# Kernel tuning notes

Measured on AMD Instinct MI355X. Metric: run time of the kernel, lower is better.

## Reference

```python
import jax, jax.numpy as jnp
import numpy as np

# ---- Clifford algebra Cl(3,0): 8 blades ordered by grade: [1, e1,e2,e3, e12,e13,e23, e123] ----
_ORDER = [0, 1, 2, 4, 3, 5, 6, 7]  # bitmask of each blade in grade-sorted order
GRADES = np.array([0, 1, 1, 1, 2, 2, 2, 3])  # grade (subspace) of each blade
EPS = 1e-6

def _build_cayley():
    C = np.zeros((8, 8, 8), np.float32)
    for ia, a in enumerate(_ORDER):
        for ib, b in enumerate(_ORDER):
            # reordering sign from anticommuting basis vectors (Euclidean metric -> squares +1)
            t, tot = a >> 1, 0
            while t:
                tot += bin(t & b).count("1")
                t >>= 1
            s = 1.0 if tot % 2 == 0 else -1.0
            C[ia, ib, _ORDER.index(a ^ b)] = s
    return jnp.asarray(C)

CAYLEY = _build_cayley()  # [8,8,8], highly sparse (64 nonzeros)

def mvlinear(x, W, b):
    # x: [B,N,Cin,8], W: [Cout,Cin,4] per-grade weights, b: [Cout] bias on scalar blade
    Wf = W[:, :, GRADES]                               # [Cout,Cin,8] via repeat over grades [1,3,3,1]
    y = jnp.einsum("bnci,oci->bnoi", x, Wf)
    return y.at[..., 0].add(b)

def setup_inputs() -> dict:
    key = jax.random.key(0)
    ks = jax.random.split(key, 5)
    B, N, Cin, Ch = 8, 4096, 64, 128
    return {
        "x": jax.random.normal(ks[0], (B, N, Cin, 8), jnp.float32),
        "W1": jax.random.normal(ks[1], (Ch, Cin, 4), jnp.float32) / np.sqrt(Cin),
        "b1": jax.random.normal(ks[2], (Ch,), jnp.float32) * 0.02,
        "W2": jax.random.normal(ks[3], (Cin, Ch, 4), jnp.float32) / np.sqrt(Ch),
        "b2": jax.random.normal(ks[4], (Cin,), jnp.float32) * 0.02,
        "a": jnp.ones((Cin,), jnp.float32),
    }

def reference(x, W1, b1, W2, b2, a):
    h = mvlinear(x, W1, b1)                                   # [B,N,Ch,8]
    h = jnp.einsum("bnci,ijk,bncj->bnck", h, CAYLEY, h)       # geometric product (sparse Cayley)
    y = mvlinear(h, W2, b2)                                   # [B,N,Cin,8]
    # MVLayerNorm: per-channel multivector norm (Euclidean: sqrt(sum of squares)),
    # averaged over channels, then scale by learned a
    norm = jnp.sqrt(jnp.sum(y * y, axis=-1, keepdims=True))   # [B,N,Cin,1]
    denom = jnp.mean(norm, axis=-2, keepdims=True) + EPS      # [B,N,1,1]
    return a[None, None, :, None] * y / denom
```

## Files before the change

### kernel.cpp

```cpp
#include <hip/hip_runtime.h>
#include <stdint.h>

typedef unsigned short u16;
typedef __attribute__((ext_vector_type(4))) float f32x4;
typedef __attribute__((ext_vector_type(8))) __bf16 bf16x8;

#define XPITCH 72
#define GPITCH 136

struct Cay { int idx[8][8]; float sgn[8][8]; };
constexpr int kOrder[8] = {0,1,2,4,3,5,6,7};
constexpr int ordpos(int m){ int r=-1; for(int i=0;i<8;i++) if(kOrder[i]==m) r=i; return r; }
constexpr Cay make_cay(){
  Cay c{};
  for(int ia=0; ia<8; ia++) for(int ib=0; ib<8; ib++){
    int a=kOrder[ia], b=kOrder[ib];
    int t=a>>1, tot=0;
    while(t){ int x=t&b; while(x){ tot+=x&1; x>>=1; } t>>=1; }
    c.idx[ia][ib]=ordpos(a^b);
    c.sgn[ia][ib]=(tot&1)?-1.0f:1.0f;
  }
  return c;
}
constexpr Cay CAY = make_cay();

__device__ __forceinline__ u16 f2bf(float f){
  union { float f; uint32_t u; } v; v.f=f;
  uint32_t u=v.u;
  return (u16)((u + 0x7fffu + ((u>>16)&1u)) >> 16);
}

__global__ void gp_prepack(const float* __restrict__ W1, const float* __restrict__ W2,
                           u16* __restrict__ w1p, u16* __restrict__ w2p)
{
  int t = blockIdx.x*256 + threadIdx.x;
  int e = t & 7, l = (t>>3)&63, f = t>>9;
  int lm = l & 15, lh = l >> 4;
  if (f < 64) {
    int g = f >> 4, ks = (f>>3)&1, ot = f&7;
    int o = ot*16 + lm, c = ks*32 + lh*8 + e;
    w1p[f*512 + l*8 + e] = f2bf(W1[(o*64 + c)*4 + g]);
  } else {
    int f2 = f - 64;
    int g = f2 >> 4, ks = (f2>>2)&3, ot = f2&3;
    int outc = ot*16 + lm, o = ks*32 + lh*8 + e;
    w2p[f2*512 + l*8 + e] = f2bf(W2[(outc*128 + o)*4 + g]);
  }
}

__global__ __launch_bounds__(512,4) void gp_fused(
    const float* __restrict__ x, const u16* __restrict__ w1p,
    const float* __restrict__ b1, const u16* __restrict__ w2p,
    const float* __restrict__ b2, const float* __restrict__ avec,
    float* __restrict__ out)
{
  __shared__ u16 SH[8*32*GPITCH];
  __shared__ float redArr[32][4];
  __shared__ float denomArr[32];

  const int tid = threadIdx.x;
  const int w  = tid >> 6;
  const int l  = tid & 63;
  const int lm = l & 15;
  const int lh = l >> 4;

  {
    const float4* x4 = reinterpret_cast<const float4*>(x) + (size_t)blockIdx.x * 4096;
    #pragma unroll
    for (int it = 0; it < 8; ++it) {
      int q = it*512 + tid;
      float4 v = x4[q];
      int i0 = (q & 1) * 4;
      int c  = (q >> 1) & 63;
      int p  = q >> 7;
      SH[((i0+0)*32 + p)*XPITCH + c] = f2bf(v.x);
      SH[((i0+1)*32 + p)*XPITCH + c] = f2bf(v.y);
      SH[((i0+2)*32 + p)*XPITCH + c] = f2bf(v.z);
      SH[((i0+3)*32 + p)*XPITCH + c] = f2bf(v.w);
    }
  }
  __syncthreads();

  constexpr int BSTART[4] = {0,1,4,7};
  constexpr int BCNT[4]   = {1,3,3,1};

  f32x4 acc1[2][8];
  #pragma unroll
  for (int pt=0; pt<2; ++pt)
    #pragma unroll
    for (int b=0; b<8; ++b)
      acc1[pt][b] = (f32x4){0.f,0.f,0.f,0.f};

  const uint4* w1f = reinterpret_cast<const uint4*>(w1p);
  #pragma unroll
  for (int g=0; g<4; ++g) {
    #pragma unroll
    for (int ks=0; ks<2; ++ks) {
      uint4 bu = w1f[(((g*2+ks)*8 + w)*64) + l];
      bf16x8 bv = __builtin_bit_cast(bf16x8, bu);
      #pragma unroll
      for (int bi=0; bi<3; ++bi) {
        if (bi >= BCNT[g]) break;
        const int blade = BSTART[g] + bi;
        #pragma unroll
        for (int pt=0; pt<2; ++pt) {
          uint4 au = *reinterpret_cast<const uint4*>(
              &SH[((blade*32 + pt*16 + lm)*XPITCH) + ks*32 + lh*8]);
          bf16x8 av = __builtin_bit_cast(bf16x8, au);
          acc1[pt][blade] = __builtin_amdgcn_mfma_f32_16x16x32_bf16(av, bv, acc1[pt][blade], 0,0,0);
        }
      }
    }
  }
  __syncthreads();

  {
    const float b1v = b1[w*16 + lm];
    #pragma unroll
    for (int pt=0; pt<2; ++pt) {
      #pragma unroll
      for (int r=0; r<4; ++r) {
        float h[8];
        #pragma unroll
        for (int b=0; b<8; ++b) h[b] = acc1[pt][b][r];
        h[0] += b1v;
        float gg[8] = {0,0,0,0,0,0,0,0};
        #pragma unroll
        for (int i=0; i<8; ++i)
          #pragma unroll
          for (int j=0; j<8; ++j)
            gg[CAY.idx[i][j]] += CAY.sgn[i][j] * h[i] * h[j];
        const int pos = pt*16 + lh*4 + r;
        #pragma unroll
        for (int b=0; b<8; ++b)
          SH[(b*32 + pos)*GPITCH + w*16 + lm] = f2bf(gg[b]);
      }
    }
  }
  __syncthreads();

  const int pt2 = w >> 2;
  const int ot2 = w & 3;
  f32x4 acc2[8];
  #pragma unroll
  for (int b=0; b<8; ++b) acc2[b] = (f32x4){0.f,0.f,0.f,0.f};

  const uint4* w2f = reinterpret_cast<const uint4*>(w2p);
  #pragma unroll
  for (int ks=0; ks<4; ++ks) {
    #pragma unroll
    for (int g=0; g<4; ++g) {
      uint4 bu = w2f[(((g*4+ks)*4 + ot2)*64) + l];
      bf16x8 bv = __builtin_bit_cast(bf16x8, bu);
      #pragma unroll
      for (int bi=0; bi<3; ++bi) {
        if (bi >= BCNT[g]) break;
        const int blade = BSTART[g] + bi;
        uint4 au = *reinterpret_cast<const uint4*>(
            &SH[((blade*32 + pt2*16 + lm)*GPITCH) + ks*32 + lh*8]);
        bf16x8 av = __builtin_bit_cast(bf16x8, au);
        acc2[blade] = __builtin_amdgcn_mfma_f32_16x16x32_bf16(av, bv, acc2[blade], 0,0,0);
      }
    }
  }

  const float b2v  = b2[ot2*16 + lm];
  const float aval = avec[ot2*16 + lm];
  #pragma unroll
  for (int r=0; r<4; ++r) acc2[0][r] += b2v;

  float nrm[4];
  #pragma unroll
  for (int r=0; r<4; ++r) {
    float s = 0.f;
    #pragma unroll
    for (int b=0; b<8; ++b) s += acc2[b][r]*acc2[b][r];
    nrm[r] = sqrtf(s);
  }
  #pragma unroll
  for (int r=0; r<4; ++r) {
    float v = nrm[r];
    v += __shfl_xor(v, 1, 64);
    v += __shfl_xor(v, 2, 64);
    v += __shfl_xor(v, 4, 64);
    v += __shfl_xor(v, 8, 64);
    nrm[r] = v;
  }
  if (lm == 0) {
    #pragma unroll
    for (int r=0; r<4; ++r) redArr[pt2*16 + lh*4 + r][ot2] = nrm[r];
  }
  __syncthreads();
  if (tid < 32)
    denomArr[tid] = (redArr[tid][0]+redArr[tid][1]+redArr[tid][2]+redArr[tid][3])
                    * (1.0f/64.0f) + 1e-6f;
  __syncthreads();

  #pragma unroll
  for (int r=0; r<4; ++r) {
    const int pos = pt2*16 + lh*4 + r;
    const float sc = aval / denomArr[pos];
    float4 o0, o1;
    o0.x = acc2[0][r]*sc; o0.y = acc2[1][r]*sc; o0.z = acc2[2][r]*sc; o0.w = acc2[3][r]*sc;
    o1.x = acc2[4][r]*sc; o1.y = acc2[5][r]*sc; o1.z = acc2[6][r]*sc; o1.w = acc2[7][r]*sc;
    size_t P = (size_t)blockIdx.x*32 + pos;
    float4* op = reinterpret_cast<float4*>(out + (P*64 + (size_t)(ot2*16+lm))*8);
    op[0] = o0; op[1] = o1;
  }
}

extern "C" void kernel_launch(void* const* d_in, const int* in_sizes, int n_in,
                              void* d_out, int out_size, void* d_ws, size_t ws_size,
                              hipStream_t stream)
{
  const float* x  = (const float*)d_in[0];
  const float* W1 = (const float*)d_in[1];
  const float* b1 = (const float*)d_in[2];
  const float* W2 = (const float*)d_in[3];
  const float* b2 = (const float*)d_in[4];
  const float* a  = (const float*)d_in[5];
  float* out = (float*)d_out;

  u16* w1p = (u16*)d_ws;
  u16* w2p = w1p + 32768;

  gp_prepack<<<256, 256, 0, stream>>>(W1, W2, w1p, w2p);
  gp_fused<<<1024, 512, 0, stream>>>(x, w1p, b1, w2p, b2, a, out);
}
```

Before: 47.87 us.

## Halve block tile to 16 points, XOR-swizzle LDS, symmetric geometric product

Each block now handles 16 points with 256 threads instead of 32 points with 512, and the grid doubles to compensate. The padded LDS pitches are replaced with an XOR-swizzled layout. The first GEMM is transposed so one LDS activation fragment feeds two MFMAs with different weight tiles. The geometric product exploits symmetric Cayley pairs to cut multiply count, and bf16 conversion uses packed v_cvt_pk_bf16_f32 with vectorized LDS stores. These changes target LDS bank conflicts, conversion overhead and ALU work in the Cayley step, at the cost of smaller tiles and more per-block weight reloads.

```diff
diff --git a/kernel.cpp b/kernel.cpp
--- a/kernel.cpp
+++ b/kernel.cpp
@@ -4,9 +4,6 @@
 typedef unsigned short u16;
 typedef __attribute__((ext_vector_type(4))) float f32x4;
 typedef __attribute__((ext_vector_type(8))) __bf16 bf16x8;
-
-#define XPITCH 72
-#define GPITCH 136
 
 struct Cay { int idx[8][8]; float sgn[8][8]; };
 constexpr int kOrder[8] = {0,1,2,4,3,5,6,7};
@@ -24,10 +21,41 @@
 }
 constexpr Cay CAY = make_cay();
 
+struct GPTab { float dsgn[8]; int np; int pi[28]; int pj[28]; int pk[28]; float ps[28]; };
+constexpr GPTab make_gptab(){
+  GPTab t{};
+  for (int i=0;i<8;i++) t.dsgn[i] = CAY.sgn[i][i];
+  t.np = 0;
+  for (int i=0;i<8;i++) for (int j=i+1;j<8;j++){
+    float s = CAY.sgn[i][j] + CAY.sgn[j][i];
+    if (s != 0.0f){ t.pi[t.np]=i; t.pj[t.np]=j; t.pk[t.np]=CAY.idx[i][j]; t.ps[t.np]=s; t.np++; }
+  }
+  return t;
+}
+constexpr GPTab GPT = make_gptab();
+
+__device__ __forceinline__ void gprod(const float* h, float* g){
+  float g0 = h[0]*h[0];
+  #pragma unroll
+  for (int i=1;i<8;i++) g0 = fmaf(GPT.dsgn[i]>0.f ? h[i] : -h[i], h[i], g0);
+  g[0] = g0;
+  #pragma unroll
+  for (int k=1;k<8;k++) g[k] = 0.f;
+  #pragma unroll
+  for (int t=0;t<GPT.np;t++)
+    g[GPT.pk[t]] = fmaf(GPT.ps[t]*h[GPT.pi[t]], h[GPT.pj[t]], g[GPT.pk[t]]);
+}
+
 __device__ __forceinline__ u16 f2bf(float f){
   union { float f; uint32_t u; } v; v.f=f;
   uint32_t u=v.u;
   return (u16)((u + 0x7fffu + ((u>>16)&1u)) >> 16);
+}
+
+__device__ __forceinline__ uint32_t cvtpk(float lo, float hi){
+  uint32_t r;
+  asm("v_cvt_pk_bf16_f32 %0, %1, %2" : "=v"(r) : "v"(lo), "v"(hi));
+  return r;
 }
 
 __global__ void gp_prepack(const float* __restrict__ W1, const float* __restrict__ W2,
@@ -48,35 +76,39 @@
   }
 }
 
-__global__ __launch_bounds__(512,4) void gp_fused(
+__global__ __launch_bounds__(256,4) void gp_fused(
     const float* __restrict__ x, const u16* __restrict__ w1p,
     const float* __restrict__ b1, const u16* __restrict__ w2p,
     const float* __restrict__ b2, const float* __restrict__ avec,
     float* __restrict__ out)
 {
-  __shared__ u16 SH[8*32*GPITCH];
-  __shared__ float redArr[32][4];
-  __shared__ float denomArr[32];
+  __shared__ __align__(16) char SH[32768];
+  __shared__ float redArr[16][4];
+  __shared__ float denomArr[16];
 
   const int tid = threadIdx.x;
   const int w  = tid >> 6;
   const int l  = tid & 63;
   const int lm = l & 15;
   const int lh = l >> 4;
+  const int xk = (lm & 7) << 4;
 
   {
-    const float4* x4 = reinterpret_cast<const float4*>(x) + (size_t)blockIdx.x * 4096;
-    #pragma unroll
-    for (int it = 0; it < 8; ++it) {
-      int q = it*512 + tid;
-      float4 v = x4[q];
-      int i0 = (q & 1) * 4;
-      int c  = (q >> 1) & 63;
-      int p  = q >> 7;
-      SH[((i0+0)*32 + p)*XPITCH + c] = f2bf(v.x);
-      SH[((i0+1)*32 + p)*XPITCH + c] = f2bf(v.y);
-      SH[((i0+2)*32 + p)*XPITCH + c] = f2bf(v.z);
-      SH[((i0+3)*32 + p)*XPITCH + c] = f2bf(v.w);
+    const int cp = tid & 31;
+    const int pr = tid >> 5;
+    const float4* xt = reinterpret_cast<const float4*>(x) + (size_t)blockIdx.x * 2048;
+    #pragma unroll
+    for (int it=0; it<2; ++it){
+      const int p = pr + it*8;
+      const float4* src = xt + p*128 + cp*4;
+      float4 v0 = src[0], v1 = src[1], v2 = src[2], v3 = src[3];
+      uint32_t pk[8];
+      pk[0]=cvtpk(v0.x,v2.x); pk[1]=cvtpk(v0.y,v2.y); pk[2]=cvtpk(v0.z,v2.z); pk[3]=cvtpk(v0.w,v2.w);
+      pk[4]=cvtpk(v1.x,v3.x); pk[5]=cvtpk(v1.y,v3.y); pk[6]=cvtpk(v1.z,v3.z); pk[7]=cvtpk(v1.w,v3.w);
+      const int xo = (p & 7) << 4;
+      #pragma unroll
+      for (int b=0;b<8;b++)
+        *reinterpret_cast<uint32_t*>(SH + ((((p*8+b)<<7) + (cp<<2)) ^ xo)) = pk[b];
     }
   }
   __syncthreads();
@@ -86,86 +118,96 @@
 
   f32x4 acc1[2][8];
   #pragma unroll
-  for (int pt=0; pt<2; ++pt)
+  for (int cc=0; cc<2; ++cc)
     #pragma unroll
     for (int b=0; b<8; ++b)
-      acc1[pt][b] = (f32x4){0.f,0.f,0.f,0.f};
+      acc1[cc][b] = (f32x4){0.f,0.f,0.f,0.f};
 
   const uint4* w1f = reinterpret_cast<const uint4*>(w1p);
   #pragma unroll
-  for (int g=0; g<4; ++g) {
-    #pragma unroll
-    for (int ks=0; ks<2; ++ks) {
-      uint4 bu = w1f[(((g*2+ks)*8 + w)*64) + l];
-      bf16x8 bv = __builtin_bit_cast(bf16x8, bu);
-      #pragma unroll
-      for (int bi=0; bi<3; ++bi) {
-        if (bi >= BCNT[g]) break;
-        const int blade = BSTART[g] + bi;
-        #pragma unroll
-        for (int pt=0; pt<2; ++pt) {
-          uint4 au = *reinterpret_cast<const uint4*>(
-              &SH[((blade*32 + pt*16 + lm)*XPITCH) + ks*32 + lh*8]);
-          bf16x8 av = __builtin_bit_cast(bf16x8, au);
-          acc1[pt][blade] = __builtin_amdgcn_mfma_f32_16x16x32_bf16(av, bv, acc1[pt][blade], 0,0,0);
-        }
-      }
-    }
-  }
-  __syncthreads();
-
-  {
-    const float b1v = b1[w*16 + lm];
-    #pragma unroll
-    for (int pt=0; pt<2; ++pt) {
-      #pragma unroll
-      for (int r=0; r<4; ++r) {
+  for (int g4=0; g4<4; ++g4){
+    #pragma unroll
+    for (int ks=0; ks<2; ++ks){
+      uint4 wa = w1f[((g4*2+ks)*8 + w    )*64 + l];
+      uint4 wb = w1f[((g4*2+ks)*8 + w + 4)*64 + l];
+      bf16x8 wav = __builtin_bit_cast(bf16x8, wa);
+      bf16x8 wbv = __builtin_bit_cast(bf16x8, wb);
+      #pragma unroll
+      for (int bi=0; bi<3; ++bi){
+        if (bi >= BCNT[g4]) break;
+        const int blade = BSTART[g4] + bi;
+        bf16x8 xv = *reinterpret_cast<const bf16x8*>(
+            SH + ((((lm*8+blade)<<7) + ((ks*32+lh*8)<<1)) ^ xk));
+        acc1[0][blade] = __builtin_amdgcn_mfma_f32_16x16x32_bf16(wav, xv, acc1[0][blade], 0,0,0);
+        acc1[1][blade] = __builtin_amdgcn_mfma_f32_16x16x32_bf16(wbv, xv, acc1[1][blade], 0,0,0);
+      }
+    }
+  }
+  __syncthreads();
+
+  #pragma unroll
+  for (int cc=0; cc<2; ++cc){
+    const int cht = w + cc*4;
+    const float4 b14 = reinterpret_cast<const float4*>(b1)[cht*4 + lh];
+    const float bb[4] = {b14.x, b14.y, b14.z, b14.w};
+    uint32_t lo[8], hi[8];
+    #pragma unroll
+    for (int rp=0; rp<2; ++rp){
+      float ga[8], gb[8];
+      {
         float h[8];
         #pragma unroll
-        for (int b=0; b<8; ++b) h[b] = acc1[pt][b][r];
-        h[0] += b1v;
-        float gg[8] = {0,0,0,0,0,0,0,0};
+        for (int b=0;b<8;b++) h[b] = acc1[cc][b][rp*2+0];
+        h[0] += bb[rp*2+0];
+        gprod(h, ga);
+      }
+      {
+        float h[8];
         #pragma unroll
-        for (int i=0; i<8; ++i)
-          #pragma unroll
-          for (int j=0; j<8; ++j)
-            gg[CAY.idx[i][j]] += CAY.sgn[i][j] * h[i] * h[j];
-        const int pos = pt*16 + lh*4 + r;
-        #pragma unroll
-        for (int b=0; b<8; ++b)
-          SH[(b*32 + pos)*GPITCH + w*16 + lm] = f2bf(gg[b]);
-      }
-    }
-  }
-  __syncthreads();
-
-  const int pt2 = w >> 2;
-  const int ot2 = w & 3;
+        for (int b=0;b<8;b++) h[b] = acc1[cc][b][rp*2+1];
+        h[0] += bb[rp*2+1];
+        gprod(h, gb);
+      }
+      #pragma unroll
+      for (int b=0;b<8;b++){
+        uint32_t v = cvtpk(ga[b], gb[b]);
+        if (rp==0) lo[b] = v; else hi[b] = v;
+      }
+    }
+    const int chByte = (cht*16 + lh*4) << 1;
+    #pragma unroll
+    for (int b=0;b<8;b++){
+      uint2 v; v.x = lo[b]; v.y = hi[b];
+      *reinterpret_cast<uint2*>(SH + ((((lm*8+b)<<8) + chByte) ^ xk)) = v;
+    }
+  }
+  __syncthreads();
+
   f32x4 acc2[8];
   #pragma unroll
   for (int b=0; b<8; ++b) acc2[b] = (f32x4){0.f,0.f,0.f,0.f};
 
   const uint4* w2f = reinterpret_cast<const uint4*>(w2p);
   #pragma unroll
-  for (int ks=0; ks<4; ++ks) {
-    #pragma unroll
-    for (int g=0; g<4; ++g) {
-      uint4 bu = w2f[(((g*4+ks)*4 + ot2)*64) + l];
-      bf16x8 bv = __builtin_bit_cast(bf16x8, bu);
-      #pragma unroll
-      for (int bi=0; bi<3; ++bi) {
-        if (bi >= BCNT[g]) break;
-        const int blade = BSTART[g] + bi;
-        uint4 au = *reinterpret_cast<const uint4*>(
-            &SH[((blade*32 + pt2*16 + lm)*GPITCH) + ks*32 + lh*8]);
-        bf16x8 av = __builtin_bit_cast(bf16x8, au);
-        acc2[blade] = __builtin_amdgcn_mfma_f32_16x16x32_bf16(av, bv, acc2[blade], 0,0,0);
-      }
-    }
-  }
-
-  const float b2v  = b2[ot2*16 + lm];
-  const float aval = avec[ot2*16 + lm];
+  for (int ks=0; ks<4; ++ks){
+    #pragma unroll
+    for (int g4=0; g4<4; ++g4){
+      uint4 wu = w2f[((g4*4+ks)*4 + w)*64 + l];
+      bf16x8 wv = __builtin_bit_cast(bf16x8, wu);
+      #pragma unroll
+      for (int bi=0; bi<3; ++bi){
+        if (bi >= BCNT[g4]) break;
+        const int blade = BSTART[g4] + bi;
+        bf16x8 gv = *reinterpret_cast<const bf16x8*>(
+            SH + ((((lm*8+blade)<<8) + ((ks*32+lh*8)<<1)) ^ xk));
+        acc2[blade] = __builtin_amdgcn_mfma_f32_16x16x32_bf16(gv, wv, acc2[blade], 0,0,0);
+      }
+    }
+  }
+
+  const int oc = w*16 + lm;
+  const float b2v  = b2[oc];
+  const float aval = avec[oc];
   #pragma unroll
   for (int r=0; r<4; ++r) acc2[0][r] += b2v;
 
@@ -174,7 +216,7 @@
   for (int r=0; r<4; ++r) {
     float s = 0.f;
     #pragma unroll
-    for (int b=0; b<8; ++b) s += acc2[b][r]*acc2[b][r];
+    for (int b=0; b<8; ++b) s = fmaf(acc2[b][r], acc2[b][r], s);
     nrm[r] = sqrtf(s);
   }
   #pragma unroll
@@ -188,23 +230,23 @@
   }
   if (lm == 0) {
     #pragma unroll
-    for (int r=0; r<4; ++r) redArr[pt2*16 + lh*4 + r][ot2] = nrm[r];
-  }
-  __syncthreads();
-  if (tid < 32)
+    for (int r=0; r<4; ++r) redArr[lh*4 + r][w] = nrm[r];
+  }
+  __syncthreads();
+  if (tid < 16)
     denomArr[tid] = (redArr[tid][0]+redArr[tid][1]+redArr[tid][2]+redArr[tid][3])
                     * (1.0f/64.0f) + 1e-6f;
   __syncthreads();
 
   #pragma unroll
   for (int r=0; r<4; ++r) {
-    const int pos = pt2*16 + lh*4 + r;
+    const int pos = lh*4 + r;
     const float sc = aval / denomArr[pos];
     float4 o0, o1;
     o0.x = acc2[0][r]*sc; o0.y = acc2[1][r]*sc; o0.z = acc2[2][r]*sc; o0.w = acc2[3][r]*sc;
     o1.x = acc2[4][r]*sc; o1.y = acc2[5][r]*sc; o1.z = acc2[6][r]*sc; o1.w = acc2[7][r]*sc;
-    size_t P = (size_t)blockIdx.x*32 + pos;
-    float4* op = reinterpret_cast<float4*>(out + (P*64 + (size_t)(ot2*16+lm))*8);
+    size_t P = (size_t)blockIdx.x*16 + pos;
+    float4* op = reinterpret_cast<float4*>(out + (P*64 + (size_t)oc)*8);
     op[0] = o0; op[1] = o1;
   }
 }
@@ -225,5 +267,5 @@
   u16* w2p = w1p + 32768;
 
   gp_prepack<<<256, 256, 0, stream>>>(W1, W2, w1p, w2p);
-  gp_fused<<<1024, 512, 0, stream>>>(x, w1p, b1, w2p, b2, a, out);
-}
+  gp_fused<<<2048, 256, 0, stream>>>(x, w1p, b1, w2p, b2, a, out);
+}
```

After: 43.84 us. 1.09x faster.
